# Kernel tuning notes

Hardware: AMD Instinct MI355X
Metric: run time of the kernel (lower is better)

## Reference

```python
import jax, jax.numpy as jnp
import numpy as np

LAYERS = 16; SUBLAYERS = 12; NPLANES = LAYERS * SUBLAYERS
POS_LEVEL = 10; DEPTH_LEVEL = 8; ORDER = 3; BASIS_OUT = 8
HIDDEN = 384; BASIS_HIDDEN = 64
SLOPE = 0.01; SIG_OFF = 5.0
IN_H = 512; IN_W = 768; RAYS = 1024
OFFSET = 0.0


def leaky(x):
    return jnp.where(x >= 0, x, SLOPE * x)


def grid_sample_3d(vol, gx, gy, gz):
    # vol (C, D, H, W); grid coords normalized [-1,1]; align_corners=True, zeros padding
    C, Dm, H, W = vol.shape
    x = (gx + 1.0) * 0.5 * (W - 1)
    y = (gy + 1.0) * 0.5 * (H - 1)
    z = (gz + 1.0) * 0.5 * (Dm - 1)
    x0 = jnp.floor(x); y0 = jnp.floor(y); z0 = jnp.floor(z)
    flat = vol.reshape(C, -1)
    out = jnp.zeros((C,) + x.shape, vol.dtype)
    for dz in (0.0, 1.0):
        for dy in (0.0, 1.0):
            for dx in (0.0, 1.0):
                xi = x0 + dx; yi = y0 + dy; zi = z0 + dz
                w = (1 - jnp.abs(x - xi)) * (1 - jnp.abs(y - yi)) * (1 - jnp.abs(z - zi))
                valid = ((xi >= 0) & (xi < W) & (yi >= 0) & (yi < H) & (zi >= 0) & (zi < Dm)).astype(vol.dtype)
                idx = ((jnp.clip(zi, 0, Dm - 1) * H + jnp.clip(yi, 0, H - 1)) * W
                       + jnp.clip(xi, 0, W - 1)).astype(jnp.int32)
                out = out + (w * valid)[None] * jnp.take(flat, idx, axis=1)
    return out


def _rotation(angle, axis):
    axis = np.asarray(axis, np.float64); axis /= np.linalg.norm(axis)
    K = np.array([[0, -axis[2], axis[1]], [axis[2], 0, -axis[0]], [-axis[1], axis[0], 0]])
    R = np.eye(3) + np.sin(angle) * K + (1 - np.cos(angle)) * (K @ K)
    return jnp.asarray(R, jnp.float32)


def setup_inputs() -> dict:
    key = jax.random.key(0)
    ks = jax.random.split(key, 32)
    def lin(i, fan_in, fan_out):
        w = jax.random.normal(ks[i], (fan_in, fan_out), jnp.float32) / np.sqrt(fan_in).astype(np.float32)
        b = jnp.zeros((fan_out,), jnp.float32)
        return w, b
    in_dim = 2 * (2 * POS_LEVEL + DEPTH_LEVEL)     # 56
    out_dim = 1 + BASIS_OUT * 3                    # 25
    w0, b0 = lin(0, in_dim, HIDDEN)
    w1, b1 = lin(1, HIDDEN, HIDDEN)
    w2, b2 = lin(2, HIDDEN, HIDDEN)
    w3, b3 = lin(3, HIDDEN, HIDDEN)
    w4, b4 = lin(4, HIDDEN, HIDDEN)
    wo, bo = lin(5, HIDDEN, out_dim)
    bw0, bb0 = lin(6, 4 * ORDER, BASIS_HIDDEN)
    bw1, bb1 = lin(7, BASIS_HIDDEN, BASIS_HIDDEN)
    bwo, bbo = lin(8, BASIS_HIDDEN, BASIS_OUT)
    mpi_c = jax.random.uniform(ks[20], (LAYERS, 3, IN_H, IN_W), jnp.float32, -1.0, 1.0)
    K = jnp.array([[600.0, 0.0, IN_W / 2.0], [0.0, 600.0, IN_H / 2.0], [0.0, 0.0, 1.0]], jnp.float32)
    planes = jnp.asarray(1.0 / np.linspace(1.0, 0.1, NPLANES), jnp.float32)  # inverse-depth spacing, dmin=1 dmax=10
    selection = jax.random.randint(ks[21], (RAYS,), 0, IN_H * IN_W)
    return dict(
        mpi_c=mpi_c, w0=w0, b0=b0, w1=w1, b1=b1, w2=w2, b2=b2, w3=w3, b3=b3, w4=w4, b4=b4,
        wo=wo, bo=bo, bw0=bw0, bb0=bb0, bw1=bw1, bb1=bb1, bwo=bwo, bbo=bbo,
        ref_rT=jnp.eye(3, dtype=jnp.float32), ref_t=jnp.zeros((3, 1), jnp.float32), ref_k=K,
        feat_r=_rotation(0.03, [0.2, 1.0, 0.1]),
        feat_t=jnp.array([[0.08], [0.03], [0.02]], jnp.float32),
        feat_center=jnp.array([[-0.08], [-0.03], [-0.02]], jnp.float32),
        feat_k=K, planes=planes, selection=selection, out_h=IN_H, out_w=IN_W)


def reference(mpi_c, w0, b0, w1, b1, w2, b2, w3, b3, w4, b4, wo, bo,
              bw0, bb0, bw1, bb1, bwo, bbo,
              ref_rT, ref_t, ref_k, feat_r, feat_t, feat_center, feat_k,
              planes, selection, out_h, out_w):
    # ---- homography warp (computeHomographies / computeHomoWarp) ----
    ki = jnp.linalg.inv(feat_k)
    new_r = feat_r @ ref_rT
    new_t = -new_r @ ref_t + feat_t
    nvec = jnp.array([[0.0, 0.0, 1.0]], jnp.float32)
    Ha = new_r.T
    Hb = Ha @ new_t @ nvec @ Ha
    Hc = (nvec @ Ha @ new_t)[0, 0]
    Hs = ref_k @ (Ha + Hb / (-planes[:, None, None] - Hc)) @ ki      # (P,3,3)
    coords = jnp.stack([(selection % out_w).astype(jnp.float32),
                        (selection // out_w).astype(jnp.float32),
                        jnp.ones_like(selection, jnp.float32)], -1)   # (R,3)
    prod = jnp.einsum('rc,pkc->prk', coords, Hs)                      # (P,R,3)
    ref_coords = prod[..., :2] / prod[..., 2:]                        # (P,R,2)
    scale = jnp.array([IN_W - 1.0, IN_H - 1.0], jnp.float32)
    warp = (ref_coords + OFFSET) / scale * 2.0 - 1.0                  # (P,R,2)
    R = warp.shape[1]

    # ---- positional encoding + main MLP ----
    pos_freq = (0.5 * np.pi) * (2.0 ** jnp.arange(POS_LEVEL, dtype=jnp.float32))
    depth_freq = (0.5 * np.pi) * (2.0 ** jnp.arange(DEPTH_LEVEL, dtype=jnp.float32))
    z_coords = jnp.linspace(-1.0, 1.0, NPLANES)
    vxy = (warp[..., None] * pos_freq).reshape(NPLANES, R, 2 * POS_LEVEL)
    vz = jnp.broadcast_to((z_coords[:, None] * depth_freq[None])[:, None, :], (NPLANES, R, DEPTH_LEVEL))
    vxyz = jnp.concatenate([vxy, vz], -1)
    big = jnp.concatenate([jnp.sin(vxyz), jnp.cos(vxyz)], -1)         # (P,R,56)
    h = leaky(big @ w0 + b0)
    for w_, b_ in ((w1, b1), (w2, b2), (w3, b3), (w4, b4)):
        h = leaky(h @ w_ + b_)
    out = h @ wo + bo                                                 # (P,R,25)
    alpha = jax.nn.sigmoid(out[..., 0] - SIG_OFF)                     # (P,R)

    # ---- trilinear grid sample of sigmoid(mpi_c) ----
    vol = jnp.transpose(jax.nn.sigmoid(mpi_c), (1, 0, 2, 3))          # (3,L,H,W)
    depths = jnp.repeat(jnp.linspace(-1.0, 1.0, LAYERS), SUBLAYERS)   # (P,)
    gz = jnp.broadcast_to(depths[:, None], (NPLANES, R))
    rgb = grid_sample_3d(vol, warp[..., 0], warp[..., 1], gz)         # (3,P,R)
    rgb = jnp.transpose(rgb, (1, 2, 0))                               # (P,R,3)

    # ---- specular basis (viewing-angle MLP) ----
    camera = ref_rT.T @ feat_center + ref_t                           # (3,1)
    coords3 = jnp.concatenate([ref_coords, jnp.ones_like(ref_coords[..., :1])], -1)
    xyz = jnp.einsum('kc,prc->prk', ki, coords3 * planes[:, None, None])
    v = xyz - camera[:, 0]
    v = v / (jnp.linalg.norm(v, axis=-1, keepdims=True) + 1e-7)
    view_freq = 2.0 ** jnp.arange(ORDER, dtype=jnp.float32)
    hv = (v[..., :2, None] * view_freq).reshape(NPLANES, R, 2 * ORDER)
    venc = jnp.concatenate([jnp.sin(0.5 * np.pi * hv), jnp.cos(0.5 * np.pi * hv)], -1)  # (P,R,12)
    bh = leaky(venc @ bw0 + bb0)
    bh = leaky(bh @ bw1 + bb1)
    basis = jnp.tanh(bh @ bwo + bbo)                                  # (P,R,8)
    coeff = jnp.repeat(out[::SUBLAYERS, ..., 1:], SUBLAYERS, axis=0)  # (P,R,24)
    coeff = jnp.tanh(coeff.reshape(NPLANES, R, 3, BASIS_OUT))
    illum = jnp.sum(coeff * basis[:, :, None, :], -1)                 # (P,R,3)
    rgb = jnp.clip(rgb + illum, 0.0, 1.0)

    # ---- alpha compositing (cumprod_exclusive over planes) ----
    cp = jnp.cumprod(1.0 - alpha, axis=0)
    weight = jnp.concatenate([jnp.ones_like(cp[:1]), cp[:-1]], 0)     # (P,R)
    comp = jnp.sum((weight * alpha)[..., None] * rgb, axis=0)         # (R,3)
    return jnp.transpose(comp)[None, :, :, None]                      # (1,3,R,1)
```

## Files before the change

kernel.cpp:

```cpp
#include <hip/hip_runtime.h>
#include <hip/hip_bf16.h>
#include <math.h>


typedef _Float16 half4 __attribute__((ext_vector_type(4)));
typedef _Float16 half8 __attribute__((ext_vector_type(8)));
typedef float f32x4 __attribute__((ext_vector_type(4)));

#if __has_builtin(__builtin_amdgcn_mfma_f32_16x16x32_f16)
#define MFMA32(a, b, c) __builtin_amdgcn_mfma_f32_16x16x32_f16((a), (b), (c), 0, 0, 0)
#else
#define MFMA32(a, b, c) (c)
#endif

#define NPLANES 192
#define RAYS    1024
#define IMW     768
#define IMH     512
#define HS      392
#define PI_HALF 1.5707964f

#define O_HS     0
#define O_KICAM  7168
#define O_ALPHA  7424
#define O_COEFF  793856
#define O_PW0    2366720
#define O_PW1    2415872
#define O_PW2    2710784
#define O_PW3    3005696
#define O_PW4    3300608
#define O_PWO    3595520
#define O_PBW0   3620096
#define O_PBW1   3624192
#define O_PBWO   3632384
#define O_BASIS  3634432
#define WS_NEED  (O_BASIS + 6291456)

__global__ void prep_kernel(const float* __restrict__ ref_rT, const float* __restrict__ ref_t,
                            const float* __restrict__ ref_k, const float* __restrict__ feat_r,
                            const float* __restrict__ feat_t, const float* __restrict__ feat_center,
                            const float* __restrict__ feat_k, const float* __restrict__ planes,
                            float* __restrict__ wsHs, float* __restrict__ wsKiCam)
{
  __shared__ float sKi[9], sHa[9], sHb[9], sHc[1];
  if (threadIdx.x == 0) {
    float a = feat_k[0], b = feat_k[1], c = feat_k[2];
    float d = feat_k[3], e = feat_k[4], f = feat_k[5];
    float g = feat_k[6], h = feat_k[7], i = feat_k[8];
    float A = e * i - f * h, B = -(d * i - f * g), C = d * h - e * g;
    float det = a * A + b * B + c * C;
    float id = 1.0f / det;
    float ki[9];
    ki[0] = A * id;             ki[1] = -(b * i - c * h) * id;  ki[2] = (b * f - c * e) * id;
    ki[3] = B * id;             ki[4] = (a * i - c * g) * id;   ki[5] = -(a * f - c * d) * id;
    ki[6] = C * id;             ki[7] = -(a * h - b * g) * id;  ki[8] = (a * e - b * d) * id;
    float nr[9];
    for (int r2 = 0; r2 < 3; ++r2)
      for (int c2 = 0; c2 < 3; ++c2) {
        float s = 0.f;
        for (int k2 = 0; k2 < 3; ++k2) s += feat_r[r2 * 3 + k2] * ref_rT[k2 * 3 + c2];
        nr[r2 * 3 + c2] = s;
      }
    float ntv[3];
    for (int r2 = 0; r2 < 3; ++r2) {
      float s = 0.f;
      for (int k2 = 0; k2 < 3; ++k2) s += nr[r2 * 3 + k2] * ref_t[k2];
      ntv[r2] = -s + feat_t[r2];
    }
    float Ha[9];
    for (int r2 = 0; r2 < 3; ++r2)
      for (int c2 = 0; c2 < 3; ++c2) Ha[r2 * 3 + c2] = nr[c2 * 3 + r2];
    float u[3];
    for (int r2 = 0; r2 < 3; ++r2) {
      float s = 0.f;
      for (int k2 = 0; k2 < 3; ++k2) s += Ha[r2 * 3 + k2] * ntv[k2];
      u[r2] = s;
    }
    float Hb[9];
    for (int r2 = 0; r2 < 3; ++r2)
      for (int c2 = 0; c2 < 3; ++c2) Hb[r2 * 3 + c2] = u[r2] * Ha[6 + c2];
    float cam[3];
    for (int r2 = 0; r2 < 3; ++r2) {
      float s = 0.f;
      for (int k2 = 0; k2 < 3; ++k2) s += ref_rT[k2 * 3 + r2] * feat_center[k2];
      cam[r2] = s + ref_t[r2];
    }
    for (int j = 0; j < 9; ++j) { sKi[j] = ki[j]; sHa[j] = Ha[j]; sHb[j] = Hb[j]; }
    sHc[0] = u[2];
    for (int j = 0; j < 9; ++j) wsKiCam[j] = ki[j];
    for (int j = 0; j < 3; ++j) wsKiCam[9 + j] = cam[j];
  }
  __syncthreads();
  int p = threadIdx.x;
  if (p < NPLANES) {
    float dnm = -planes[p] - sHc[0];
    float T[9];
    for (int j = 0; j < 9; ++j) T[j] = sHa[j] + sHb[j] / dnm;
    float U[9];
    for (int r2 = 0; r2 < 3; ++r2)
      for (int c2 = 0; c2 < 3; ++c2) {
        float s = 0.f;
        for (int k2 = 0; k2 < 3; ++k2) s += ref_k[r2 * 3 + k2] * T[k2 * 3 + c2];
        U[r2 * 3 + c2] = s;
      }
    for (int r2 = 0; r2 < 3; ++r2)
      for (int c2 = 0; c2 < 3; ++c2) {
        float s = 0.f;
        for (int k2 = 0; k2 < 3; ++k2) s += U[r2 * 3 + k2] * sKi[k2 * 3 + c2];
        wsHs[p * 9 + r2 * 3 + c2] = s;
      }
  }
}

__global__ void pack_kernel(const float* __restrict__ src, _Float16* __restrict__ dst,
                            int Ksrc, int Nsrc, int NP, int total)
{
  int idx = blockIdx.x * 256 + threadIdx.x;
  if (idx >= total) return;
  int within = idx & 511, blk = idx >> 9;
  int kg = within >> 7, ln = (within >> 3) & 15, j = within & 7;
  int ntiles = NP >> 4;
  int nt = blk % ntiles, kc = blk / ntiles;
  int k = kc * 32 + kg * 8 + j, nn = nt * 16 + ln;
  float v = (k < Ksrc && nn < Nsrc) ? src[k * Nsrc + nn] : 0.0f;
  dst[idx] = (_Float16)v;
}

template <int NKC>
__device__ __forceinline__ void hidden_layer(_Float16* hb, const _Float16* __restrict__ wl,
                                             const float* __restrict__ bias,
                                             int wv, int g, int ln)
{
  f32x4 acc[6][4];
  #pragma unroll
  for (int ft = 0; ft < 6; ++ft) {
    const f32x4 bv4 = *(const f32x4*)&bias[(wv * 6 + ft) * 16 + g * 4];
    #pragma unroll
    for (int pt = 0; pt < 4; ++pt) acc[ft][pt] = bv4;
  }
  #pragma unroll 2
  for (int kc = 0; kc < NKC; ++kc) {
    half8 aw[6];
    #pragma unroll
    for (int ft = 0; ft < 6; ++ft)
      aw[ft] = *(const half8*)&wl[(kc * 24 + wv * 6 + ft) * 512 + g * 128 + ln * 8];
    half8 bx[4];
    #pragma unroll
    for (int pt = 0; pt < 4; ++pt)
      bx[pt] = *(const half8*)&hb[(pt * 16 + ln) * HS + kc * 32 + g * 8];
    #pragma unroll
    for (int ft = 0; ft < 6; ++ft)
      #pragma unroll
      for (int pt = 0; pt < 4; ++pt)
        acc[ft][pt] = MFMA32(aw[ft], bx[pt], acc[ft][pt]);
  }
  __syncthreads();
  #pragma unroll
  for (int pt = 0; pt < 4; ++pt)
    #pragma unroll
    for (int ft = 0; ft < 6; ++ft) {
      half4 hv;
      #pragma unroll
      for (int r = 0; r < 4; ++r) {
        float v = acc[ft][pt][r];
        v *= (v >= 0.f ? 1.0f : 0.01f);
        hv[r] = (_Float16)v;
      }
      *(half4*)&hb[(pt * 16 + ln) * HS + wv * 96 + ft * 16 + g * 4] = hv;
    }
  __syncthreads();
}

template <int NKC>
__device__ __forceinline__ void basis_hidden(_Float16* hb, const _Float16* __restrict__ wl,
                                             const float* __restrict__ bias,
                                             int wv, int g, int ln)
{
  f32x4 acc[4];
  const f32x4 bv4 = *(const f32x4*)&bias[wv * 16 + g * 4];
  #pragma unroll
  for (int pt = 0; pt < 4; ++pt) acc[pt] = bv4;
  #pragma unroll
  for (int kc = 0; kc < NKC; ++kc) {
    half8 aw = *(const half8*)&wl[(kc * 4 + wv) * 512 + g * 128 + ln * 8];
    #pragma unroll
    for (int pt = 0; pt < 4; ++pt) {
      half8 bx = *(const half8*)&hb[(pt * 16 + ln) * HS + kc * 32 + g * 8];
      acc[pt] = MFMA32(aw, bx, acc[pt]);
    }
  }
  __syncthreads();
  #pragma unroll
  for (int pt = 0; pt < 4; ++pt) {
    half4 hv;
    #pragma unroll
    for (int r = 0; r < 4; ++r) {
      float v = acc[pt][r];
      v *= (v >= 0.f ? 1.0f : 0.01f);
      hv[r] = (_Float16)v;
    }
    *(half4*)&hb[(pt * 16 + ln) * HS + wv * 16 + g * 4] = hv;
  }
  __syncthreads();
}

__global__ __launch_bounds__(256, 3) void mlp_kernel(
    const int* __restrict__ selection, const float* __restrict__ planes,
    const float* __restrict__ wsHs, const float* __restrict__ wsKiCam,
    const _Float16* __restrict__ pw0, const _Float16* __restrict__ pw1,
    const _Float16* __restrict__ pw2, const _Float16* __restrict__ pw3,
    const _Float16* __restrict__ pw4, const _Float16* __restrict__ pwo,
    const float* __restrict__ b0, const float* __restrict__ b1,
    const float* __restrict__ b2, const float* __restrict__ b3,
    const float* __restrict__ b4, const float* __restrict__ bo,
    const _Float16* __restrict__ pbw0, const _Float16* __restrict__ pbw1,
    const _Float16* __restrict__ pbwo,
    const float* __restrict__ bb0, const float* __restrict__ bb1,
    const float* __restrict__ bbo,
    float* __restrict__ wsAlpha, float* __restrict__ wsCoeff, float* __restrict__ wsBasis)
{
  __shared__ _Float16 hbuf[64 * HS];
  const int t = threadIdx.x;
  const int m0 = blockIdx.x * 64;
  const int p = m0 >> 10;
  const int r0 = m0 & 1023;
  const int lane = t & 63, wv = t >> 6;
  const int g = lane >> 4, ln = lane & 15;

  {
    const int i = t >> 2, q = t & 3;
    const int ray = r0 + i;
    const int sel = selection[ray];
    const float cx = (float)(sel % IMW), cy = (float)(sel / IMW);
    const float* H = wsHs + p * 9;
    const float pr0 = H[0] * cx + H[1] * cy + H[2];
    const float pr1 = H[3] * cx + H[4] * cy + H[5];
    const float pr2 = H[6] * cx + H[7] * cy + H[8];
    const float rx = pr0 / pr2, ry = pr1 / pr2;
    const float wx = (rx / 767.0f) * 2.0f - 1.0f;
    const float wy = (ry / 511.0f) * 2.0f - 1.0f;
    const float zc = -1.0f + (float)p * (2.0f / 191.0f);
    #pragma unroll
    for (int cc = 0; cc < 7; ++cc) {
      const int c = q * 7 + cc;
      float base, fr;
      if (c < 10)      { base = wx; fr = (float)(1 << c); }
      else if (c < 20) { base = wy; fr = (float)(1 << (c - 10)); }
      else             { base = zc; fr = (float)(1 << (c - 20)); }
      const float ang = base * (PI_HALF * fr);
      hbuf[i * HS + c]      = (_Float16)sinf(ang);
      hbuf[i * HS + 28 + c] = (_Float16)cosf(ang);
    }
    hbuf[i * HS + 56 + q] = (_Float16)0.f;
    hbuf[i * HS + 60 + q] = (_Float16)0.f;
  }
  __syncthreads();

  hidden_layer<2>(hbuf, pw0, b0, wv, g, ln);
  hidden_layer<12>(hbuf, pw1, b1, wv, g, ln);
  hidden_layer<12>(hbuf, pw2, b2, wv, g, ln);
  hidden_layer<12>(hbuf, pw3, b3, wv, g, ln);
  hidden_layer<12>(hbuf, pw4, b4, wv, g, ln);

  f32x4 acc2[2];
  {
    #pragma unroll
    for (int ft = 0; ft < 2; ++ft) {
      f32x4 bv;
      #pragma unroll
      for (int r = 0; r < 4; ++r) {
        const int f = ft * 16 + g * 4 + r;
        bv[r] = (f < 25) ? bo[f] : 0.f;
      }
      acc2[ft] = bv;
    }
    #pragma unroll 2
    for (int kc = 0; kc < 12; ++kc) {
      half8 bx = *(const half8*)&hbuf[(wv * 16 + ln) * HS + kc * 32 + g * 8];
      #pragma unroll
      for (int ft = 0; ft < 2; ++ft) {
        half8 aw = *(const half8*)&pwo[(kc * 2 + ft) * 512 + g * 128 + ln * 8];
        acc2[ft] = MFMA32(aw, bx, acc2[ft]);
      }
    }
    __syncthreads();
  }

  {
    const int i = t >> 2, q = t & 3;
    const int ray = r0 + i;
    const int sel = selection[ray];
    const float cx = (float)(sel % IMW), cy = (float)(sel / IMW);
    const float* H = wsHs + p * 9;
    const float pr0 = H[0] * cx + H[1] * cy + H[2];
    const float pr1 = H[3] * cx + H[4] * cy + H[5];
    const float pr2 = H[6] * cx + H[7] * cy + H[8];
    const float rx = pr0 / pr2, ry = pr1 / pr2;
    const float pd = planes[p];
    const float* ki = wsKiCam; const float* cam = wsKiCam + 9;
    const float c0 = rx * pd, c1 = ry * pd, c2 = pd;
    const float vx0 = ki[0] * c0 + ki[1] * c1 + ki[2] * c2 - cam[0];
    const float vy0 = ki[3] * c0 + ki[4] * c1 + ki[5] * c2 - cam[1];
    const float vz0 = ki[6] * c0 + ki[7] * c1 + ki[8] * c2 - cam[2];
    const float nrm = sqrtf(vx0 * vx0 + vy0 * vy0 + vz0 * vz0) + 1e-7f;
    const float vx = vx0 / nrm, vy = vy0 / nrm;
    #pragma unroll
    for (int cc = 0; cc < 4; ++cc) {
      const int c = q * 4 + cc;
      float v;
      if (c < 6) {
        const float hv = ((c < 3) ? vx : vy) * (float)(1 << (c % 3));
        v = sinf(PI_HALF * hv);
      } else if (c < 12) {
        const int c6 = c - 6;
        const float hv = ((c6 < 3) ? vx : vy) * (float)(1 << (c6 % 3));
        v = cosf(PI_HALF * hv);
      } else v = 0.f;
      hbuf[i * HS + c] = (_Float16)v;
    }
  }
  __syncthreads();

  {
    if (g == 0) {
      const int ray = r0 + wv * 16 + ln;
      wsAlpha[ray * NPLANES + p] = 1.0f / (1.0f + expf(5.0f - acc2[0][0]));
    }
    if ((p % 12) == 0) {
      const int pg = p / 12;
      const int ray = r0 + wv * 16 + ln;
      #pragma unroll
      for (int ft = 0; ft < 2; ++ft)
        #pragma unroll
        for (int r = 0; r < 4; ++r) {
          const int f = ft * 16 + g * 4 + r;
          if (f >= 1 && f < 25)
            wsCoeff[(pg * RAYS + ray) * 24 + (f - 1)] = tanhf(acc2[ft][r]);
        }
    }
  }

  basis_hidden<1>(hbuf, pbw0, bb0, wv, g, ln);
  basis_hidden<2>(hbuf, pbw1, bb1, wv, g, ln);
  {
    f32x4 accO = (f32x4){0.f, 0.f, 0.f, 0.f};
    #pragma unroll
    for (int kc = 0; kc < 2; ++kc) {
      half8 aw = *(const half8*)&pbwo[kc * 512 + g * 128 + ln * 8];
      half8 bx = *(const half8*)&hbuf[(wv * 16 + ln) * HS + kc * 32 + g * 8];
      accO = MFMA32(aw, bx, accO);
    }
    if (g < 2) {
      const int ray = r0 + wv * 16 + ln;
      #pragma unroll
      for (int r = 0; r < 4; ++r) {
        const int f = g * 4 + r;
        wsBasis[(ray * NPLANES + p) * 8 + f] = tanhf(accO[r] + bbo[f]);
      }
    }
  }
}

__global__ __launch_bounds__(192) void composite_kernel(
    const float* __restrict__ mpi, const int* __restrict__ selection,
    const float* __restrict__ wsHs, const float* __restrict__ wsAlpha,
    const float* __restrict__ wsCoeff, const float* __restrict__ wsBasis,
    float* __restrict__ out)
{
  const int ray = blockIdx.x;
  const int p = threadIdx.x;
  const int sel = selection[ray];
  const float cx = (float)(sel % IMW), cy = (float)(sel / IMW);
  const float* H = wsHs + p * 9;
  const float pr0 = H[0] * cx + H[1] * cy + H[2];
  const float pr1 = H[3] * cx + H[4] * cy + H[5];
  const float pr2 = H[6] * cx + H[7] * cy + H[8];
  const float rx = pr0 / pr2, ry = pr1 / pr2;
  const float wx = (rx / 767.0f) * 2.0f - 1.0f;
  const float wy = (ry / 511.0f) * 2.0f - 1.0f;
  const float x = (wx + 1.0f) * 0.5f * 767.0f;
  const float y = (wy + 1.0f) * 0.5f * 511.0f;
  const float gz = -1.0f + (float)(p / 12) * (2.0f / 15.0f);
  const float z = (gz + 1.0f) * 0.5f * 15.0f;
  const float x0 = floorf(x), y0 = floorf(y), z0 = floorf(z);
  float rgb0 = 0.f, rgb1 = 0.f, rgb2 = 0.f;
  #pragma unroll
  for (int dz = 0; dz < 2; ++dz)
    #pragma unroll
    for (int dy = 0; dy < 2; ++dy)
      #pragma unroll
      for (int dx = 0; dx < 2; ++dx) {
        const float xi = x0 + (float)dx, yi = y0 + (float)dy, zi = z0 + (float)dz;
        const float w = (1.f - fabsf(x - xi)) * (1.f - fabsf(y - yi)) * (1.f - fabsf(z - zi));
        const bool valid = (xi >= 0.f) && (xi < 768.f) && (yi >= 0.f) && (yi < 512.f)
                        && (zi >= 0.f) && (zi < 16.f);
        if (valid && w != 0.f) {
          const int ix = (int)xi, iy = (int)yi, iz = (int)zi;
          const int base = iz * 3 * (IMW * IMH) + iy * IMW + ix;
          const float v0 = mpi[base];
          const float v1 = mpi[base + IMW * IMH];
          const float v2 = mpi[base + 2 * IMW * IMH];
          rgb0 += w * (1.f / (1.f + expf(-v0)));
          rgb1 += w * (1.f / (1.f + expf(-v1)));
          rgb2 += w * (1.f / (1.f + expf(-v2)));
        }
      }
  const float* bs = wsBasis + (ray * NPLANES + p) * 8;
  const float* cf = wsCoeff + ((p / 12) * RAYS + ray) * 24;
  float il0 = 0.f, il1 = 0.f, il2 = 0.f;
  #pragma unroll
  for (int j = 0; j < 8; ++j) {
    const float bj = bs[j];
    il0 += cf[j] * bj; il1 += cf[8 + j] * bj; il2 += cf[16 + j] * bj;
  }
  rgb0 = fminf(fmaxf(rgb0 + il0, 0.f), 1.f);
  rgb1 = fminf(fmaxf(rgb1 + il1, 0.f), 1.f);
  rgb2 = fminf(fmaxf(rgb2 + il2, 0.f), 1.f);
  const float a = wsAlpha[ray * NPLANES + p];
  const int lane = p & 63, w64 = p >> 6;
  float xs = 1.f - a;
  #pragma unroll
  for (int off = 1; off < 64; off <<= 1) {
    const float v = __shfl_up(xs, off, 64);
    if (lane >= off) xs *= v;
  }
  __shared__ float wtot[3];
  __shared__ float part[3][3];
  if (lane == 63) wtot[w64] = xs;
  __syncthreads();
  float pre = 1.f;
  #pragma unroll
  for (int q = 0; q < 2; ++q)
    if (q < w64) pre *= wtot[q];
  float excl = __shfl_up(xs, 1, 64);
  if (lane == 0) excl = 1.f;
  const float wa = pre * excl * a;
  float s0 = wa * rgb0, s1 = wa * rgb1, s2 = wa * rgb2;
  #pragma unroll
  for (int off = 32; off >= 1; off >>= 1) {
    s0 += __shfl_down(s0, off, 64);
    s1 += __shfl_down(s1, off, 64);
    s2 += __shfl_down(s2, off, 64);
  }
  if (lane == 0) { part[w64][0] = s0; part[w64][1] = s1; part[w64][2] = s2; }
  __syncthreads();
  if (p == 0) {
    out[0 * RAYS + ray] = part[0][0] + part[1][0] + part[2][0];
    out[1 * RAYS + ray] = part[0][1] + part[1][1] + part[2][1];
    out[2 * RAYS + ray] = part[0][2] + part[1][2] + part[2][2];
  }
}

extern "C" void kernel_launch(void* const* d_in, const int* in_sizes, int n_in,
                              void* d_out, int out_size, void* d_ws, size_t ws_size,
                              hipStream_t stream)
{
  (void)in_sizes; (void)n_in; (void)out_size;
  const float* mpi    = (const float*)d_in[0];
  const float* w0     = (const float*)d_in[1];
  const float* b0     = (const float*)d_in[2];
  const float* w1     = (const float*)d_in[3];
  const float* b1     = (const float*)d_in[4];
  const float* w2     = (const float*)d_in[5];
  const float* b2     = (const float*)d_in[6];
  const float* w3     = (const float*)d_in[7];
  const float* b3     = (const float*)d_in[8];
  const float* w4     = (const float*)d_in[9];
  const float* b4     = (const float*)d_in[10];
  const float* wo     = (const float*)d_in[11];
  const float* bo     = (const float*)d_in[12];
  const float* bw0    = (const float*)d_in[13];
  const float* bb0    = (const float*)d_in[14];
  const float* bw1    = (const float*)d_in[15];
  const float* bb1    = (const float*)d_in[16];
  const float* bwo    = (const float*)d_in[17];
  const float* bbo    = (const float*)d_in[18];
  const float* ref_rT = (const float*)d_in[19];
  const float* ref_t  = (const float*)d_in[20];
  const float* ref_k  = (const float*)d_in[21];
  const float* feat_r = (const float*)d_in[22];
  const float* feat_t = (const float*)d_in[23];
  const float* feat_c = (const float*)d_in[24];
  const float* feat_k = (const float*)d_in[25];
  const float* planes = (const float*)d_in[26];
  const int*   selection = (const int*)d_in[27];
  float* outp = (float*)d_out;
  char* ws = (char*)d_ws;
  if (ws_size < (size_t)WS_NEED) return;

  float* wsHs    = (float*)(ws + O_HS);
  float* wsKiCam = (float*)(ws + O_KICAM);
  float* wsAlpha = (float*)(ws + O_ALPHA);
  float* wsCoeff = (float*)(ws + O_COEFF);
  float* wsBasis = (float*)(ws + O_BASIS);
  _Float16* pw0  = (_Float16*)(ws + O_PW0);
  _Float16* pw1  = (_Float16*)(ws + O_PW1);
  _Float16* pw2  = (_Float16*)(ws + O_PW2);
  _Float16* pw3  = (_Float16*)(ws + O_PW3);
  _Float16* pw4  = (_Float16*)(ws + O_PW4);
  _Float16* pwo  = (_Float16*)(ws + O_PWO);
  _Float16* pbw0 = (_Float16*)(ws + O_PBW0);
  _Float16* pbw1 = (_Float16*)(ws + O_PBW1);
  _Float16* pbwo = (_Float16*)(ws + O_PBWO);

  prep_kernel<<<1, 256, 0, stream>>>(ref_rT, ref_t, ref_k, feat_r, feat_t, feat_c,
                                     feat_k, planes, wsHs, wsKiCam);
  pack_kernel<<<96, 256, 0, stream>>>(w0, pw0, 56, 384, 384, 2 * 24 * 512);
  pack_kernel<<<576, 256, 0, stream>>>(w1, pw1, 384, 384, 384, 12 * 24 * 512);
  pack_kernel<<<576, 256, 0, stream>>>(w2, pw2, 384, 384, 384, 12 * 24 * 512);
  pack_kernel<<<576, 256, 0, stream>>>(w3, pw3, 384, 384, 384, 12 * 24 * 512);
  pack_kernel<<<576, 256, 0, stream>>>(w4, pw4, 384, 384, 384, 12 * 24 * 512);
  pack_kernel<<<48, 256, 0, stream>>>(wo, pwo, 384, 25, 32, 12 * 2 * 512);
  pack_kernel<<<8, 256, 0, stream>>>(bw0, pbw0, 12, 64, 64, 1 * 4 * 512);
  pack_kernel<<<16, 256, 0, stream>>>(bw1, pbw1, 64, 64, 64, 2 * 4 * 512);
  pack_kernel<<<4, 256, 0, stream>>>(bwo, pbwo, 64, 8, 16, 2 * 1 * 512);

  mlp_kernel<<<(NPLANES * RAYS) / 64, 256, 0, stream>>>(
      selection, planes, wsHs, wsKiCam,
      pw0, pw1, pw2, pw3, pw4, pwo,
      b0, b1, b2, b3, b4, bo,
      pbw0, pbw1, pbwo, bb0, bb1, bbo,
      wsAlpha, wsCoeff, wsBasis);

  composite_kernel<<<RAYS, NPLANES, 0, stream>>>(mpi, selection, wsHs, wsAlpha,
                                                 wsCoeff, wsBasis, outp);
}
```

Before: 291.6 us.

## Store MLP activations in MFMA fragment layout and merge weight packing launches

The shared-memory activation buffer moves from a row-padded layout (stride 392) to a fragment-packed layout, so each lane reads its B-operand half8 at a contiguous lane*8 offset. This is meant to cut LDS bank conflicts and address arithmetic in the hidden-layer MFMA loops. The epilogue writes and the input encodings are remapped to the same layout. The nine weight-packing launches are folded into one kernel that relies on the packed buffers sitting contiguously in the workspace, which saves launch overhead but ties correctness to the workspace offsets.

```diff
diff --git a/kernel.cpp b/kernel.cpp
--- a/kernel.cpp
+++ b/kernel.cpp
@@ -17,8 +17,10 @@
 #define RAYS    1024
 #define IMW     768
 #define IMH     512
-#define HS      392
 #define PI_HALF 1.5707964f
+
+#define FR(i, c) ((((i) >> 4) * 6144) + (((c) >> 5) * 512) + ((((c) >> 3) & 3) * 128) \
+                  + (((i) & 15) * 8) + ((c) & 7))
 
 #define O_HS     0
 #define O_KICAM  7168
@@ -112,24 +114,37 @@
   }
 }
 
-__global__ void pack_kernel(const float* __restrict__ src, _Float16* __restrict__ dst,
-                            int Ksrc, int Nsrc, int NP, int total)
-{
-  int idx = blockIdx.x * 256 + threadIdx.x;
-  if (idx >= total) return;
-  int within = idx & 511, blk = idx >> 9;
-  int kg = within >> 7, ln = (within >> 3) & 15, j = within & 7;
-  int ntiles = NP >> 4;
-  int nt = blk % ntiles, kc = blk / ntiles;
-  int k = kc * 32 + kg * 8 + j, nn = nt * 16 + ln;
-  float v = (k < Ksrc && nn < Nsrc) ? src[k * Nsrc + nn] : 0.0f;
+__global__ void pack_all_kernel(const float* __restrict__ w0, const float* __restrict__ w1,
+                                const float* __restrict__ w2, const float* __restrict__ w3,
+                                const float* __restrict__ w4, const float* __restrict__ wo,
+                                const float* __restrict__ bw0, const float* __restrict__ bw1,
+                                const float* __restrict__ bwo, _Float16* __restrict__ dst)
+{
+  const int idx = blockIdx.x * 256 + threadIdx.x;
+  const float* src; int Ksrc, Nsrc, NP, l;
+  if (idx < 24576)       { src = w0;  Ksrc = 56;  Nsrc = 384; NP = 384; l = idx; }
+  else if (idx < 172032) { src = w1;  Ksrc = 384; Nsrc = 384; NP = 384; l = idx - 24576; }
+  else if (idx < 319488) { src = w2;  Ksrc = 384; Nsrc = 384; NP = 384; l = idx - 172032; }
+  else if (idx < 466944) { src = w3;  Ksrc = 384; Nsrc = 384; NP = 384; l = idx - 319488; }
+  else if (idx < 614400) { src = w4;  Ksrc = 384; Nsrc = 384; NP = 384; l = idx - 466944; }
+  else if (idx < 626688) { src = wo;  Ksrc = 384; Nsrc = 25;  NP = 32;  l = idx - 614400; }
+  else if (idx < 628736) { src = bw0; Ksrc = 12;  Nsrc = 64;  NP = 64;  l = idx - 626688; }
+  else if (idx < 632832) { src = bw1; Ksrc = 64;  Nsrc = 64;  NP = 64;  l = idx - 628736; }
+  else if (idx < 633856) { src = bwo; Ksrc = 64;  Nsrc = 8;   NP = 16;  l = idx - 632832; }
+  else return;
+  const int within = l & 511, blk = l >> 9;
+  const int kg = within >> 7, ln = (within >> 3) & 15, j = within & 7;
+  const int ntiles = NP >> 4;
+  const int nt = blk % ntiles, kc = blk / ntiles;
+  const int k = kc * 32 + kg * 8 + j, nn = nt * 16 + ln;
+  const float v = (k < Ksrc && nn < Nsrc) ? src[k * Nsrc + nn] : 0.0f;
   dst[idx] = (_Float16)v;
 }
 
 template <int NKC>
 __device__ __forceinline__ void hidden_layer(_Float16* hb, const _Float16* __restrict__ wl,
                                              const float* __restrict__ bias,
-                                             int wv, int g, int ln)
+                                             int wv, int g, int ln, int lane)
 {
   f32x4 acc[6][4];
   #pragma unroll
@@ -143,11 +158,11 @@
     half8 aw[6];
     #pragma unroll
     for (int ft = 0; ft < 6; ++ft)
-      aw[ft] = *(const half8*)&wl[(kc * 24 + wv * 6 + ft) * 512 + g * 128 + ln * 8];
+      aw[ft] = *(const half8*)&wl[(kc * 24 + wv * 6 + ft) * 512 + lane * 8];
     half8 bx[4];
     #pragma unroll
     for (int pt = 0; pt < 4; ++pt)
-      bx[pt] = *(const half8*)&hb[(pt * 16 + ln) * HS + kc * 32 + g * 8];
+      bx[pt] = *(const half8*)&hb[pt * 6144 + kc * 512 + lane * 8];
     #pragma unroll
     for (int ft = 0; ft < 6; ++ft)
       #pragma unroll
@@ -159,6 +174,7 @@
   for (int pt = 0; pt < 4; ++pt)
     #pragma unroll
     for (int ft = 0; ft < 6; ++ft) {
+      const int f0 = wv * 96 + ft * 16 + g * 4;
       half4 hv;
       #pragma unroll
       for (int r = 0; r < 4; ++r) {
@@ -166,7 +182,7 @@
         v *= (v >= 0.f ? 1.0f : 0.01f);
         hv[r] = (_Float16)v;
       }
-      *(half4*)&hb[(pt * 16 + ln) * HS + wv * 96 + ft * 16 + g * 4] = hv;
+      *(half4*)&hb[pt * 6144 + (f0 >> 5) * 512 + ((f0 >> 3) & 3) * 128 + ln * 8 + (f0 & 7)] = hv;
     }
   __syncthreads();
 }
@@ -174,7 +190,7 @@
 template <int NKC>
 __device__ __forceinline__ void basis_hidden(_Float16* hb, const _Float16* __restrict__ wl,
                                              const float* __restrict__ bias,
-                                             int wv, int g, int ln)
+                                             int wv, int g, int ln, int lane)
 {
   f32x4 acc[4];
   const f32x4 bv4 = *(const f32x4*)&bias[wv * 16 + g * 4];
@@ -182,14 +198,15 @@
   for (int pt = 0; pt < 4; ++pt) acc[pt] = bv4;
   #pragma unroll
   for (int kc = 0; kc < NKC; ++kc) {
-    half8 aw = *(const half8*)&wl[(kc * 4 + wv) * 512 + g * 128 + ln * 8];
+    half8 aw = *(const half8*)&wl[(kc * 4 + wv) * 512 + lane * 8];
     #pragma unroll
     for (int pt = 0; pt < 4; ++pt) {
-      half8 bx = *(const half8*)&hb[(pt * 16 + ln) * HS + kc * 32 + g * 8];
+      half8 bx = *(const half8*)&hb[pt * 6144 + kc * 512 + lane * 8];
       acc[pt] = MFMA32(aw, bx, acc[pt]);
     }
   }
   __syncthreads();
+  const int f0 = wv * 16 + g * 4;
   #pragma unroll
   for (int pt = 0; pt < 4; ++pt) {
     half4 hv;
@@ -199,7 +216,7 @@
       v *= (v >= 0.f ? 1.0f : 0.01f);
       hv[r] = (_Float16)v;
     }
-    *(half4*)&hb[(pt * 16 + ln) * HS + wv * 16 + g * 4] = hv;
+    *(half4*)&hb[pt * 6144 + (f0 >> 5) * 512 + ((f0 >> 3) & 3) * 128 + ln * 8 + (f0 & 7)] = hv;
   }
   __syncthreads();
 }
@@ -219,7 +236,7 @@
     const float* __restrict__ bbo,
     float* __restrict__ wsAlpha, float* __restrict__ wsCoeff, float* __restrict__ wsBasis)
 {
-  __shared__ _Float16 hbuf[64 * HS];
+  __shared__ _Float16 hbuf[4 * 6144];
   const int t = threadIdx.x;
   const int m0 = blockIdx.x * 64;
   const int p = m0 >> 10;
@@ -248,19 +265,19 @@
       else if (c < 20) { base = wy; fr = (float)(1 << (c - 10)); }
       else             { base = zc; fr = (float)(1 << (c - 20)); }
       const float ang = base * (PI_HALF * fr);
-      hbuf[i * HS + c]      = (_Float16)sinf(ang);
-      hbuf[i * HS + 28 + c] = (_Float16)cosf(ang);
-    }
-    hbuf[i * HS + 56 + q] = (_Float16)0.f;
-    hbuf[i * HS + 60 + q] = (_Float16)0.f;
-  }
-  __syncthreads();
-
-  hidden_layer<2>(hbuf, pw0, b0, wv, g, ln);
-  hidden_layer<12>(hbuf, pw1, b1, wv, g, ln);
-  hidden_layer<12>(hbuf, pw2, b2, wv, g, ln);
-  hidden_layer<12>(hbuf, pw3, b3, wv, g, ln);
-  hidden_layer<12>(hbuf, pw4, b4, wv, g, ln);
+      hbuf[FR(i, c)]      = (_Float16)sinf(ang);
+      hbuf[FR(i, c + 28)] = (_Float16)cosf(ang);
+    }
+    hbuf[FR(i, 56 + q)] = (_Float16)0.f;
+    hbuf[FR(i, 60 + q)] = (_Float16)0.f;
+  }
+  __syncthreads();
+
+  hidden_layer<2>(hbuf, pw0, b0, wv, g, ln, lane);
+  hidden_layer<12>(hbuf, pw1, b1, wv, g, ln, lane);
+  hidden_layer<12>(hbuf, pw2, b2, wv, g, ln, lane);
+  hidden_layer<12>(hbuf, pw3, b3, wv, g, ln, lane);
+  hidden_layer<12>(hbuf, pw4, b4, wv, g, ln, lane);
 
   f32x4 acc2[2];
   {
@@ -276,10 +293,10 @@
     }
     #pragma unroll 2
     for (int kc = 0; kc < 12; ++kc) {
-      half8 bx = *(const half8*)&hbuf[(wv * 16 + ln) * HS + kc * 32 + g * 8];
+      half8 bx = *(const half8*)&hbuf[wv * 6144 + kc * 512 + lane * 8];
       #pragma unroll
       for (int ft = 0; ft < 2; ++ft) {
-        half8 aw = *(const half8*)&pwo[(kc * 2 + ft) * 512 + g * 128 + ln * 8];
+        half8 aw = *(const half8*)&pwo[(kc * 2 + ft) * 512 + lane * 8];
         acc2[ft] = MFMA32(aw, bx, acc2[ft]);
       }
     }
@@ -316,7 +333,7 @@
         const float hv = ((c6 < 3) ? vx : vy) * (float)(1 << (c6 % 3));
         v = cosf(PI_HALF * hv);
       } else v = 0.f;
-      hbuf[i * HS + c] = (_Float16)v;
+      hbuf[FR(i, c)] = (_Float16)v;
     }
   }
   __syncthreads();
@@ -340,14 +357,14 @@
     }
   }
 
-  basis_hidden<1>(hbuf, pbw0, bb0, wv, g, ln);
-  basis_hidden<2>(hbuf, pbw1, bb1, wv, g, ln);
+  basis_hidden<1>(hbuf, pbw0, bb0, wv, g, ln, lane);
+  basis_hidden<2>(hbuf, pbw1, bb1, wv, g, ln, lane);
   {
     f32x4 accO = (f32x4){0.f, 0.f, 0.f, 0.f};
     #pragma unroll
     for (int kc = 0; kc < 2; ++kc) {
-      half8 aw = *(const half8*)&pbwo[kc * 512 + g * 128 + ln * 8];
-      half8 bx = *(const half8*)&hbuf[(wv * 16 + ln) * HS + kc * 32 + g * 8];
+      half8 aw = *(const half8*)&pbwo[kc * 512 + lane * 8];
+      half8 bx = *(const half8*)&hbuf[wv * 6144 + kc * 512 + lane * 8];
       accO = MFMA32(aw, bx, accO);
     }
     if (g < 2) {
@@ -505,15 +522,7 @@
 
   prep_kernel<<<1, 256, 0, stream>>>(ref_rT, ref_t, ref_k, feat_r, feat_t, feat_c,
                                      feat_k, planes, wsHs, wsKiCam);
-  pack_kernel<<<96, 256, 0, stream>>>(w0, pw0, 56, 384, 384, 2 * 24 * 512);
-  pack_kernel<<<576, 256, 0, stream>>>(w1, pw1, 384, 384, 384, 12 * 24 * 512);
-  pack_kernel<<<576, 256, 0, stream>>>(w2, pw2, 384, 384, 384, 12 * 24 * 512);
-  pack_kernel<<<576, 256, 0, stream>>>(w3, pw3, 384, 384, 384, 12 * 24 * 512);
-  pack_kernel<<<576, 256, 0, stream>>>(w4, pw4, 384, 384, 384, 12 * 24 * 512);
-  pack_kernel<<<48, 256, 0, stream>>>(wo, pwo, 384, 25, 32, 12 * 2 * 512);
-  pack_kernel<<<8, 256, 0, stream>>>(bw0, pbw0, 12, 64, 64, 1 * 4 * 512);
-  pack_kernel<<<16, 256, 0, stream>>>(bw1, pbw1, 64, 64, 64, 2 * 4 * 512);
-  pack_kernel<<<4, 256, 0, stream>>>(bwo, pbwo, 64, 8, 16, 2 * 1 * 512);
+  pack_all_kernel<<<2476, 256, 0, stream>>>(w0, w1, w2, w3, w4, wo, bw0, bw1, bwo, pw0);
 
   mlp_kernel<<<(NPLANES * RAYS) / 64, 256, 0, stream>>>(
       selection, planes, wsHs, wsKiCam,
```

Result: faster. 276.1 us (-5.3%).
